# Performance work log

Measured on AMD Instinct MI355X. Metric: run time of the kernel, lower is better.

Reference implementation:

```python
import jax, jax.numpy as jnp
import numpy as np

# --- MLA config (DeepSeek-V3 style, scaled) ---
HIDDEN = 4096
N_HEADS = 32
Q_LORA = 1536
KV_LORA = 512
ROPE_D = 64
NOPE_D = 128
V_D = 128
Q_HEAD_D = NOPE_D + ROPE_D  # 192
EPS = 1e-6
SCALING = Q_HEAD_D ** (-0.5)
ROPE_THETA = 10000.0
B, S = 1, 2048


def rms_norm(x, w):
    var = jnp.mean(jnp.square(x.astype(jnp.float32)), axis=-1, keepdims=True)
    return (x * jax.lax.rsqrt(var + EPS)).astype(x.dtype) * w


def rotate_half(x):
    x1, x2 = jnp.split(x, 2, axis=-1)
    return jnp.concatenate([-x2, x1], axis=-1)


def apply_rope(x, cos, sin):
    # x: [B, H, S, ROPE_D]; cos/sin: [B, S, ROPE_D] -> unsqueeze head dim
    c = cos[:, None, :, :]
    s = sin[:, None, :, :]
    return x * c + rotate_half(x) * s


def setup_inputs() -> dict:
    key = jax.random.key(0)
    ks = jax.random.split(key, 8)
    hidden_states = jax.random.normal(ks[0], (B, S, HIDDEN), dtype=jnp.float32)
    # real RoPE tables
    inv_freq = 1.0 / (ROPE_THETA ** (np.arange(0, ROPE_D, 2, dtype=np.float32) / ROPE_D))
    t = np.arange(S, dtype=np.float32)
    freqs = np.outer(t, inv_freq)                      # [S, ROPE_D/2]
    emb = np.concatenate([freqs, freqs], axis=-1)      # [S, ROPE_D]
    cos = jnp.asarray(np.cos(emb))[None].repeat(B, 0)  # [B, S, ROPE_D]
    sin = jnp.asarray(np.sin(emb))[None].repeat(B, 0)
    scale = lambda fan_in: 1.0 / np.sqrt(fan_in)
    w_q_a = jax.random.normal(ks[1], (Q_LORA, HIDDEN), dtype=jnp.float32) * scale(HIDDEN)
    q_a_ln_w = jnp.ones((Q_LORA,), dtype=jnp.float32)
    w_q_b = jax.random.normal(ks[2], (N_HEADS * Q_HEAD_D, Q_LORA), dtype=jnp.float32) * scale(Q_LORA)
    w_kv_a = jax.random.normal(ks[3], (KV_LORA + ROPE_D, HIDDEN), dtype=jnp.float32) * scale(HIDDEN)
    kv_a_ln_w = jnp.ones((KV_LORA,), dtype=jnp.float32)
    w_kv_b = jax.random.normal(ks[4], (N_HEADS * (NOPE_D + V_D), KV_LORA), dtype=jnp.float32) * scale(KV_LORA)
    w_o = jax.random.normal(ks[5], (HIDDEN, N_HEADS * V_D), dtype=jnp.float32) * scale(N_HEADS * V_D)
    return {
        'hidden_states': hidden_states, 'cos': cos, 'sin': sin,
        'w_q_a': w_q_a, 'q_a_ln_w': q_a_ln_w, 'w_q_b': w_q_b,
        'w_kv_a': w_kv_a, 'kv_a_ln_w': kv_a_ln_w, 'w_kv_b': w_kv_b, 'w_o': w_o,
    }


def reference(hidden_states, cos, sin, w_q_a, q_a_ln_w, w_q_b, w_kv_a, kv_a_ln_w, w_kv_b, w_o):
    b, s, _ = hidden_states.shape
    # --- Q path: low-rank down + RMSNorm + up ---
    q_lat = rms_norm(hidden_states @ w_q_a.T, q_a_ln_w)              # [B,S,Q_LORA]
    q = (q_lat @ w_q_b.T).reshape(b, s, N_HEADS, Q_HEAD_D)
    q = q.transpose(0, 2, 1, 3)                                       # [B,H,S,Q_HEAD_D]
    q_nope, q_rot = q[..., :NOPE_D], q[..., NOPE_D:]                  # (note: source names swapped)
    # --- KV path: shared compressed latent + single rotary key ---
    ckv = hidden_states @ w_kv_a.T                                    # [B,S,KV_LORA+ROPE_D]
    k_lat, k_rot = ckv[..., :KV_LORA], ckv[..., KV_LORA:]
    kv = (rms_norm(k_lat, kv_a_ln_w) @ w_kv_b.T).reshape(b, s, N_HEADS, NOPE_D + V_D)
    kv = kv.transpose(0, 2, 1, 3)                                     # [B,H,S,NOPE_D+V_D]
    k_nope, v = kv[..., :NOPE_D], kv[..., NOPE_D:]
    k_rot = k_rot.reshape(b, 1, s, ROPE_D)                            # single rotary key head
    # --- partial RoPE on rotary slices ---
    q_rot = apply_rope(q_rot, cos, sin)
    k_rot = apply_rope(k_rot, cos, sin)
    k_rot = jnp.broadcast_to(k_rot, (b, N_HEADS, s, ROPE_D))
    query = jnp.concatenate([q_rot, q_nope], axis=-1)                 # [B,H,S,192]
    key = jnp.concatenate([k_rot, k_nope], axis=-1)                   # [B,H,S,192]
    # --- eager causal attention ---
    scores = jnp.einsum('bhqd,bhkd->bhqk', query, key) * SCALING
    causal = jnp.tril(jnp.ones((s, s), dtype=bool))
    scores = jnp.where(causal[None, None], scores, jnp.finfo(scores.dtype).min)
    probs = jax.nn.softmax(scores, axis=-1)
    attn = jnp.einsum('bhqk,bhkd->bhqd', probs, v)                    # [B,H,S,V_D]
    attn = attn.transpose(0, 2, 1, 3).reshape(b, s, N_HEADS * V_D)
    return attn @ w_o.T                                               # [B,S,HIDDEN]
```

## Files before the change

kernel.cpp:

```cpp
#include <hip/hip_runtime.h>

typedef unsigned short u16;
typedef u16 u16x4 __attribute__((ext_vector_type(4)));
typedef u16 u16x8 __attribute__((ext_vector_type(8)));
typedef float f32x4 __attribute__((ext_vector_type(4)));
typedef __bf16 bf16x8 __attribute__((ext_vector_type(8)));

#define S_LEN 2048
#define HIDDEN_D 4096
#define NHEADS 32
#define QLORA 1536
#define KVLORA 512
#define ROPED 64
#define NOPED 128
#define VDIM 128
#define QHD 192
#define SCALING_F 0.07216878364870323f

__device__ __forceinline__ u16 f2bf(float x) {
  union { float f; unsigned u; } v; v.f = x;
  unsigned r = v.u + 0x7fffu + ((v.u >> 16) & 1u);
  return (u16)(r >> 16);
}

__device__ __forceinline__ f32x4 mfma_bf16(u16x8 a, u16x8 b, f32x4 c) {
  return __builtin_amdgcn_mfma_f32_16x16x32_bf16(
      __builtin_bit_cast(bf16x8, a), __builtin_bit_cast(bf16x8, b), c, 0, 0, 0);
}

__global__ __launch_bounds__(256) void cvt_kernel(const float* __restrict__ in,
                                                  u16* __restrict__ out, int n4) {
  int i = blockIdx.x * 256 + threadIdx.x;
  if (i >= n4) return;
  f32x4 v = ((const f32x4*)in)[i];
  u16x4 o;
  o[0] = f2bf(v[0]); o[1] = f2bf(v[1]); o[2] = f2bf(v[2]); o[3] = f2bf(v[3]);
  ((u16x4*)out)[i] = o;
}

__global__ __launch_bounds__(256, 2) void gemm_kernel(
    const u16* __restrict__ A, const float* __restrict__ B, float* __restrict__ C,
    int M, int N, int K, int lda, int ldb, int ldc)
{
  __shared__ u16 sA[2][128 * 64];
  __shared__ u16 sB[2][128 * 64];
  const int tid = threadIdx.x;
  const int wid = tid >> 6, lane = tid & 63;
  const int lr = lane & 15, lg = lane >> 4;
  const int nbn = (N + 127) >> 7;
  const int bx = blockIdx.x % nbn, by = blockIdx.x / nbn;
  const int bm = by << 7, bn = bx << 7;
  const int wm = (wid >> 1) << 6, wn = (wid & 1) << 6;

  f32x4 acc[4][4] = {};
  u16x8 areg[4];
  f32x4 br0[4], br1[4];

  auto loadA = [&](int k0) {
#pragma unroll
    for (int i = 0; i < 4; ++i) {
      int chunk = i * 256 + tid;
      int row = chunk >> 3, c8 = chunk & 7;
      int gr = bm + row; if (gr >= M) gr = M - 1;
      areg[i] = *(const u16x8*)(A + (size_t)gr * lda + k0 + (c8 << 3));
    }
  };
  auto loadB = [&](int k0) {
#pragma unroll
    for (int i = 0; i < 4; ++i) {
      int chunk = i * 256 + tid;
      int n = chunk >> 3, c8 = chunk & 7;
      int gn = bn + n; if (gn >= N) gn = N - 1;
      const float* src = B + (size_t)gn * ldb + k0 + (c8 << 3);
      br0[i] = *(const f32x4*)src;
      br1[i] = *(const f32x4*)(src + 4);
    }
  };
  auto writeA = [&](int buf) {
#pragma unroll
    for (int i = 0; i < 4; ++i)
      *(u16x8*)&sA[buf][(i * 256 + tid) * 8] = areg[i];
  };
  auto writeB = [&](int buf) {
#pragma unroll
    for (int i = 0; i < 4; ++i) {
      u16x8 v;
      v[0] = f2bf(br0[i][0]); v[1] = f2bf(br0[i][1]);
      v[2] = f2bf(br0[i][2]); v[3] = f2bf(br0[i][3]);
      v[4] = f2bf(br1[i][0]); v[5] = f2bf(br1[i][1]);
      v[6] = f2bf(br1[i][2]); v[7] = f2bf(br1[i][3]);
      *(u16x8*)&sB[buf][(i * 256 + tid) * 8] = v;
    }
  };
  auto compute = [&](int buf) {
    const u16* pa = sA[buf];
    const u16* pb = sB[buf];
#pragma unroll
    for (int ks = 0; ks < 2; ++ks) {
      const int kof = ks * 32 + lg * 8;
      u16x8 av[4], bv[4];
#pragma unroll
      for (int m = 0; m < 4; ++m) av[m] = *(const u16x8*)&pa[(wm + m * 16 + lr) * 64 + kof];
#pragma unroll
      for (int n = 0; n < 4; ++n) bv[n] = *(const u16x8*)&pb[(wn + n * 16 + lr) * 64 + kof];
#pragma unroll
      for (int m = 0; m < 4; ++m)
#pragma unroll
        for (int n = 0; n < 4; ++n)
          acc[m][n] = mfma_bf16(av[m], bv[n], acc[m][n]);
    }
  };

  const int nk = K >> 6;
  loadA(0); loadB(0);
  writeA(0); writeB(0);
  __syncthreads();
  for (int t = 0; t < nk; ++t) {
    const int cur = t & 1;
    if (t + 1 < nk) { loadA((t + 1) << 6); loadB((t + 1) << 6); }
    compute(cur);
    if (t + 1 < nk) { writeA(cur ^ 1); writeB(cur ^ 1); }
    __syncthreads();
  }
#pragma unroll
  for (int m = 0; m < 4; ++m) {
    const int row0 = bm + wm + m * 16 + (lg << 2);
#pragma unroll
    for (int n = 0; n < 4; ++n) {
      const int col = bn + wn + n * 16 + lr;
      if (col < N) {
#pragma unroll
        for (int r = 0; r < 4; ++r)
          C[(size_t)(row0 + r) * ldc + col] = acc[m][n][r];
      }
    }
  }
}

__global__ __launch_bounds__(256) void rms_kernel(const float* __restrict__ X,
                                                  const float* __restrict__ w,
                                                  u16* __restrict__ out, int D) {
  const int row = blockIdx.x;
  const float* x = X + (size_t)row * D;
  __shared__ float sb[4];
  float ss = 0.f;
  for (int i = threadIdx.x * 4; i < D; i += 1024) {
    f32x4 v = *(const f32x4*)&x[i];
    ss += v[0] * v[0] + v[1] * v[1] + v[2] * v[2] + v[3] * v[3];
  }
#pragma unroll
  for (int off = 32; off >= 1; off >>= 1) ss += __shfl_xor(ss, off, 64);
  if ((threadIdx.x & 63) == 0) sb[threadIdx.x >> 6] = ss;
  __syncthreads();
  const float inv = rsqrtf((sb[0] + sb[1] + sb[2] + sb[3]) / (float)D + 1e-6f);
  u16* o = out + (size_t)row * D;
  for (int i = threadIdx.x * 4; i < D; i += 1024) {
    f32x4 v = *(const f32x4*)&x[i];
    f32x4 wv = *(const f32x4*)&w[i];
    u16x4 u;
    u[0] = f2bf(v[0] * inv * wv[0]); u[1] = f2bf(v[1] * inv * wv[1]);
    u[2] = f2bf(v[2] * inv * wv[2]); u[3] = f2bf(v[3] * inv * wv[3]);
    *(u16x4*)&o[i] = u;
  }
}

__global__ __launch_bounds__(256) void ckv_epi_kernel(const float* __restrict__ ckv,
    const float* __restrict__ w, const float* __restrict__ cosp, const float* __restrict__ sinp,
    u16* __restrict__ klatn, u16* __restrict__ krot) {
  const int s = blockIdx.x;
  const float* x = ckv + (size_t)s * 576;
  __shared__ float sb[4];
  const int i2 = threadIdx.x * 2;
  const float a = x[i2], b = x[i2 + 1];
  float ss = a * a + b * b;
#pragma unroll
  for (int off = 32; off >= 1; off >>= 1) ss += __shfl_xor(ss, off, 64);
  if ((threadIdx.x & 63) == 0) sb[threadIdx.x >> 6] = ss;
  __syncthreads();
  const float inv = rsqrtf((sb[0] + sb[1] + sb[2] + sb[3]) / 512.0f + 1e-6f);
  klatn[(size_t)s * 512 + i2]     = f2bf(a * inv * w[i2]);
  klatn[(size_t)s * 512 + i2 + 1] = f2bf(b * inv * w[i2 + 1]);
  if (threadIdx.x < 64) {
    const int d = threadIdx.x;
    const float xr = x[512 + d];
    const float rr = (d < 32) ? -x[512 + d + 32] : x[512 + d - 32];
    krot[(size_t)s * 64 + d] = f2bf(xr * cosp[s * 64 + d] + rr * sinp[s * 64 + d]);
  }
}

__global__ __launch_bounds__(256) void q_epi_kernel(const float* __restrict__ q_raw,
    const float* __restrict__ cosp, const float* __restrict__ sinp, u16* __restrict__ Qb) {
  const int s = blockIdx.x;
  const float* x = q_raw + (size_t)s * 6144;
  for (int idx = threadIdx.x; idx < 6144; idx += 256) {
    const int h = idx / 192, d = idx - h * 192;
    float v;
    if (d < 64) {
      const float xr = x[h * 192 + 128 + d];
      const float rr = (d < 32) ? -x[h * 192 + 160 + d] : x[h * 192 + 96 + d];
      v = xr * cosp[s * 64 + d] + rr * sinp[s * 64 + d];
    } else {
      v = x[h * 192 + d - 64];
    }
    Qb[((size_t)h * 2048 + s) * QHD + d] = f2bf(v * SCALING_F);
  }
}

__global__ __launch_bounds__(256) void kv_epi_kernel(const float* __restrict__ kv_raw,
    u16* __restrict__ Knope, u16* __restrict__ Vt) {
  const int h = blockIdx.x & 31, st = blockIdx.x >> 5;
  const int s0 = st << 6;
  __shared__ u16 tile[64][VDIM + 2];
  for (int i = 0; i < 32; ++i) {
    const int idx = i * 256 + threadIdx.x;
    const int r = idx >> 7, d = idx & 127;
    const float kn = kv_raw[(size_t)(s0 + r) * 8192 + h * 256 + d];
    Knope[((size_t)h * 2048 + s0 + r) * 128 + d] = f2bf(kn);
    tile[r][d] = f2bf(kv_raw[(size_t)(s0 + r) * 8192 + h * 256 + 128 + d]);
  }
  __syncthreads();
  for (int i = 0; i < 32; ++i) {
    const int idx = i * 256 + threadIdx.x;
    const int d = idx >> 6, r = idx & 63;
    Vt[((size_t)h * 128 + d) * 2048 + s0 + r] = tile[r][d];
  }
}

__global__ __launch_bounds__(256, 2) void flash_kernel(
    const u16* __restrict__ Qb, const u16* __restrict__ Krot,
    const u16* __restrict__ Knope, const u16* __restrict__ Vt,
    u16* __restrict__ attnb)
{
  const int h = blockIdx.x & 31, qt = blockIdx.x >> 5;
  const int q0 = qt << 7;
  __shared__ u16 sK[64][QHD];
  __shared__ u16 sV[VDIM][64];
  __shared__ u16 sP[4][32][64];
  const int tid = threadIdx.x;
  const int wid = tid >> 6, lane = tid & 63;
  const int lr = lane & 15, lg = lane >> 4;

  u16x8 qf[2][6];
#pragma unroll
  for (int m = 0; m < 2; ++m) {
    const int row = q0 + wid * 32 + m * 16 + lr;
#pragma unroll
    for (int kk = 0; kk < 6; ++kk)
      qf[m][kk] = *(const u16x8*)&Qb[((size_t)h * 2048 + row) * QHD + kk * 32 + lg * 8];
  }

  f32x4 acc[2][8] = {};
  float mx[2][4], ls[2][4];
#pragma unroll
  for (int m = 0; m < 2; ++m)
#pragma unroll
    for (int r = 0; r < 4; ++r) { mx[m][r] = -1e30f; ls[m][r] = 0.f; }

  const int nkv = q0 + 128;
  u16x8 kreg[6], vreg[4];

  auto loadKV = [&](int kv0) {
#pragma unroll
    for (int i = 0; i < 6; ++i) {
      const int chunk = i * 256 + tid;
      const int row = chunk / 24, cc = chunk % 24;
      const u16* src = (cc < 8)
          ? &Krot[(size_t)(kv0 + row) * 64 + cc * 8]
          : &Knope[((size_t)h * 2048 + kv0 + row) * 128 + (cc - 8) * 8];
      kreg[i] = *(const u16x8*)src;
    }
#pragma unroll
    for (int i = 0; i < 4; ++i) {
      const int chunk = i * 256 + tid;
      const int d = chunk >> 3, c = chunk & 7;
      vreg[i] = *(const u16x8*)&Vt[((size_t)h * VDIM + d) * 2048 + kv0 + c * 8];
    }
  };

  loadKV(0);
  for (int kv0 = 0; kv0 < nkv; kv0 += 64) {
    __syncthreads();
    u16* kbase = &sK[0][0];
#pragma unroll
    for (int i = 0; i < 6; ++i) *(u16x8*)&kbase[(size_t)(i * 256 + tid) * 8] = kreg[i];
    u16* vbase = &sV[0][0];
#pragma unroll
    for (int i = 0; i < 4; ++i) *(u16x8*)&vbase[(size_t)(i * 256 + tid) * 8] = vreg[i];
    __syncthreads();
    if (kv0 + 64 < nkv) loadKV(kv0 + 64);

    f32x4 sc[2][4] = {};
#pragma unroll
    for (int kk = 0; kk < 6; ++kk) {
      u16x8 bfr[4];
#pragma unroll
      for (int n = 0; n < 4; ++n) bfr[n] = *(const u16x8*)&sK[n * 16 + lr][kk * 32 + lg * 8];
#pragma unroll
      for (int m = 0; m < 2; ++m)
#pragma unroll
        for (int n = 0; n < 4; ++n)
          sc[m][n] = mfma_bf16(qf[m][kk], bfr[n], sc[m][n]);
    }

    if (kv0 + 63 > q0 + wid * 32) {
#pragma unroll
      for (int m = 0; m < 2; ++m)
#pragma unroll
        for (int n = 0; n < 4; ++n) {
          const int kv = kv0 + n * 16 + lr;
#pragma unroll
          for (int r = 0; r < 4; ++r) {
            const int rowq = q0 + wid * 32 + m * 16 + lg * 4 + r;
            if (kv > rowq) sc[m][n][r] = -1e30f;
          }
        }
    }

#pragma unroll
    for (int m = 0; m < 2; ++m) {
      float rs[4];
#pragma unroll
      for (int r = 0; r < 4; ++r) {
        float v = fmaxf(fmaxf(sc[m][0][r], sc[m][1][r]), fmaxf(sc[m][2][r], sc[m][3][r]));
#pragma unroll
        for (int off = 1; off < 16; off <<= 1) v = fmaxf(v, __shfl_xor(v, off, 64));
        const float mnew = fmaxf(mx[m][r], v);
        const float alpha = __expf(mx[m][r] - mnew);
        mx[m][r] = mnew;
        ls[m][r] *= alpha;
#pragma unroll
        for (int df = 0; df < 8; ++df) acc[m][df][r] *= alpha;
        rs[r] = 0.f;
      }
#pragma unroll
      for (int n = 0; n < 4; ++n)
#pragma unroll
        for (int r = 0; r < 4; ++r) {
          const float p = __expf(sc[m][n][r] - mx[m][r]);
          rs[r] += p;
          sP[wid][m * 16 + lg * 4 + r][n * 16 + lr] = f2bf(p);
        }
#pragma unroll
      for (int r = 0; r < 4; ++r) {
        float v = rs[r];
#pragma unroll
        for (int off = 1; off < 16; off <<= 1) v += __shfl_xor(v, off, 64);
        ls[m][r] += v;
      }
    }

#pragma unroll
    for (int ks = 0; ks < 2; ++ks) {
      u16x8 pf0 = *(const u16x8*)&sP[wid][lr][ks * 32 + lg * 8];
      u16x8 pf1 = *(const u16x8*)&sP[wid][16 + lr][ks * 32 + lg * 8];
#pragma unroll
      for (int df = 0; df < 8; ++df) {
        u16x8 vf = *(const u16x8*)&sV[df * 16 + lr][ks * 32 + lg * 8];
        acc[0][df] = mfma_bf16(pf0, vf, acc[0][df]);
        acc[1][df] = mfma_bf16(pf1, vf, acc[1][df]);
      }
    }
  }

#pragma unroll
  for (int m = 0; m < 2; ++m)
#pragma unroll
    for (int df = 0; df < 8; ++df) {
      const int col = h * 128 + df * 16 + lr;
#pragma unroll
      for (int r = 0; r < 4; ++r) {
        const int row = q0 + wid * 32 + m * 16 + lg * 4 + r;
        attnb[(size_t)row * 4096 + col] = f2bf(acc[m][df][r] / ls[m][r]);
      }
    }
}

extern "C" void kernel_launch(void* const* d_in, const int* in_sizes, int n_in,
                              void* d_out, int out_size, void* d_ws, size_t ws_size,
                              hipStream_t stream) {
  (void)in_sizes; (void)n_in; (void)out_size; (void)ws_size;
  const float* hidden  = (const float*)d_in[0];
  const float* cosp    = (const float*)d_in[1];
  const float* sinp    = (const float*)d_in[2];
  const float* w_q_a   = (const float*)d_in[3];
  const float* q_a_ln  = (const float*)d_in[4];
  const float* w_q_b   = (const float*)d_in[5];
  const float* w_kv_a  = (const float*)d_in[6];
  const float* kv_a_ln = (const float*)d_in[7];
  const float* w_kv_b  = (const float*)d_in[8];
  const float* w_o     = (const float*)d_in[9];
  float* out = (float*)d_out;

  char* p = (char*)d_ws;
  auto alloc = [&](size_t bytes) { char* r = p; p += (bytes + 255) & ~(size_t)255; return r; };
  u16* Hb    = (u16*)alloc((size_t)S_LEN * HIDDEN_D * 2);
  u16* qlatn = (u16*)alloc((size_t)S_LEN * QLORA * 2);
  u16* klatn = (u16*)alloc((size_t)S_LEN * KVLORA * 2);
  u16* krot  = (u16*)alloc((size_t)S_LEN * ROPED * 2);
  u16* Qb    = (u16*)alloc((size_t)NHEADS * S_LEN * QHD * 2);
  u16* Knope = (u16*)alloc((size_t)NHEADS * S_LEN * NOPED * 2);
  u16* Vt    = (u16*)alloc((size_t)NHEADS * VDIM * S_LEN * 2);
  u16* attnb = (u16*)alloc((size_t)S_LEN * 4096 * 2);
  float* raw = (float*)alloc((size_t)S_LEN * 8192 * 4);
  float* qlat_raw = raw;
  float* ckv_raw  = raw + (size_t)S_LEN * QLORA;
  float* q_raw    = raw;
  float* kv_raw   = raw;

  cvt_kernel<<<(S_LEN * HIDDEN_D / 4 + 255) / 256, 256, 0, stream>>>(hidden, Hb, S_LEN * HIDDEN_D / 4);
  gemm_kernel<<<16 * 12, 256, 0, stream>>>(Hb, w_q_a, qlat_raw, 2048, 1536, 4096, 4096, 4096, 1536);
  gemm_kernel<<<16 * 5, 256, 0, stream>>>(Hb, w_kv_a, ckv_raw, 2048, 576, 4096, 4096, 4096, 576);
  rms_kernel<<<2048, 256, 0, stream>>>(qlat_raw, q_a_ln, qlatn, 1536);
  ckv_epi_kernel<<<2048, 256, 0, stream>>>(ckv_raw, kv_a_ln, cosp, sinp, klatn, krot);
  gemm_kernel<<<16 * 48, 256, 0, stream>>>(qlatn, w_q_b, q_raw, 2048, 6144, 1536, 1536, 1536, 6144);
  q_epi_kernel<<<2048, 256, 0, stream>>>(q_raw, cosp, sinp, Qb);
  gemm_kernel<<<16 * 64, 256, 0, stream>>>(klatn, w_kv_b, kv_raw, 2048, 8192, 512, 512, 512, 8192);
  kv_epi_kernel<<<1024, 256, 0, stream>>>(kv_raw, Knope, Vt);
  flash_kernel<<<512, 256, 0, stream>>>(Qb, krot, Knope, Vt, attnb);
  gemm_kernel<<<16 * 32, 256, 0, stream>>>(attnb, w_o, out, 2048, 4096, 4096, 4096, 4096, 4096);
}
```

Measured before the change: 680.3 us.

## Swizzle flash-attention LDS layouts, balance causal tiles, raise MFMA priority

The K, V and P shared-memory tiles switch to flat arrays addressed with an XOR swizzle on 16-byte chunks. This is meant to remove LDS bank conflicts on the strided row reads that feed the MFMA operands. Query tiles are now assigned to blocks in a paired order (early and late tiles) so that causal work is spread more evenly across concurrently scheduled blocks. s_setprio is raised around the MFMA loops to favour matrix issue across waves, at the cost of extra index arithmetic per access.

After: 976.8 us. +43.6%, slower.

```diff
diff --git a/kernel.cpp b/kernel.cpp
--- a/kernel.cpp
+++ b/kernel.cpp
@@ -231,11 +231,14 @@
     const u16* __restrict__ Knope, const u16* __restrict__ Vt,
     u16* __restrict__ attnb)
 {
-  const int h = blockIdx.x & 31, qt = blockIdx.x >> 5;
+  const int bid = blockIdx.x;
+  const int h = bid & 31;
+  const int q8 = (bid & 255) >> 5;
+  const int qt = (bid >> 8) ? (15 - 2 * q8) : (2 * q8);
   const int q0 = qt << 7;
-  __shared__ u16 sK[64][QHD];
-  __shared__ u16 sV[VDIM][64];
-  __shared__ u16 sP[4][32][64];
+  __shared__ u16 sK[64 * QHD];
+  __shared__ u16 sV[VDIM * 64];
+  __shared__ u16 sP[4 * 32 * 64];
   const int tid = threadIdx.x;
   const int wid = tid >> 6, lane = tid & 63;
   const int lr = lane & 15, lg = lane >> 4;
@@ -244,9 +247,10 @@
 #pragma unroll
   for (int m = 0; m < 2; ++m) {
     const int row = q0 + wid * 32 + m * 16 + lr;
+    const u16* qp = &Qb[((size_t)h * 2048 + row) * QHD];
 #pragma unroll
     for (int kk = 0; kk < 6; ++kk)
-      qf[m][kk] = *(const u16x8*)&Qb[((size_t)h * 2048 + row) * QHD + kk * 32 + lg * 8];
+      qf[m][kk] = *(const u16x8*)&qp[kk * 32 + lg * 8];
   }
 
   f32x4 acc[2][8] = {};
@@ -278,29 +282,44 @@
   };
 
   loadKV(0);
+  const int pbase = wid * 8192;
   for (int kv0 = 0; kv0 < nkv; kv0 += 64) {
     __syncthreads();
-    u16* kbase = &sK[0][0];
-#pragma unroll
-    for (int i = 0; i < 6; ++i) *(u16x8*)&kbase[(size_t)(i * 256 + tid) * 8] = kreg[i];
-    u16* vbase = &sV[0][0];
-#pragma unroll
-    for (int i = 0; i < 4; ++i) *(u16x8*)&vbase[(size_t)(i * 256 + tid) * 8] = vreg[i];
+#pragma unroll
+    for (int i = 0; i < 6; ++i) {
+      const int chunk = i * 256 + tid;
+      const int row = chunk / 24, cc = chunk % 24;
+      int b = row * 384 + cc * 16; b ^= (row & 7) << 4;
+      *(u16x8*)&sK[b >> 1] = kreg[i];
+    }
+#pragma unroll
+    for (int i = 0; i < 4; ++i) {
+      const int chunk = i * 256 + tid;
+      const int row = chunk >> 3, cc = chunk & 7;
+      int b = row * 128 + cc * 16; b ^= (row & 7) << 4;
+      *(u16x8*)&sV[b >> 1] = vreg[i];
+    }
     __syncthreads();
     if (kv0 + 64 < nkv) loadKV(kv0 + 64);
 
     f32x4 sc[2][4] = {};
+    __builtin_amdgcn_s_setprio(1);
 #pragma unroll
     for (int kk = 0; kk < 6; ++kk) {
       u16x8 bfr[4];
 #pragma unroll
-      for (int n = 0; n < 4; ++n) bfr[n] = *(const u16x8*)&sK[n * 16 + lr][kk * 32 + lg * 8];
+      for (int n = 0; n < 4; ++n) {
+        const int row = n * 16 + lr;
+        int b = row * 384 + kk * 64 + lg * 16; b ^= (row & 7) << 4;
+        bfr[n] = *(const u16x8*)&sK[b >> 1];
+      }
 #pragma unroll
       for (int m = 0; m < 2; ++m)
 #pragma unroll
         for (int n = 0; n < 4; ++n)
           sc[m][n] = mfma_bf16(qf[m][kk], bfr[n], sc[m][n]);
     }
+    __builtin_amdgcn_s_setprio(0);
 
     if (kv0 + 63 > q0 + wid * 32) {
 #pragma unroll
@@ -338,7 +357,9 @@
         for (int r = 0; r < 4; ++r) {
           const float p = __expf(sc[m][n][r] - mx[m][r]);
           rs[r] += p;
-          sP[wid][m * 16 + lg * 4 + r][n * 16 + lr] = f2bf(p);
+          const int prow = m * 16 + lg * 4 + r;
+          int b = prow * 128 + (n * 16 + lr) * 2; b ^= (prow & 7) << 4;
+          sP[(wid * 4096 + b) >> 1] = f2bf(p);
         }
 #pragma unroll
       for (int r = 0; r < 4; ++r) {
@@ -349,17 +370,23 @@
       }
     }
 
+    __builtin_amdgcn_s_setprio(1);
 #pragma unroll
     for (int ks = 0; ks < 2; ++ks) {
-      u16x8 pf0 = *(const u16x8*)&sP[wid][lr][ks * 32 + lg * 8];
-      u16x8 pf1 = *(const u16x8*)&sP[wid][16 + lr][ks * 32 + lg * 8];
+      int b0 = lr * 128 + ks * 64 + lg * 16; b0 ^= (lr & 7) << 4;
+      int b1 = (16 + lr) * 128 + ks * 64 + lg * 16; b1 ^= (lr & 7) << 4;
+      u16x8 pf0 = *(const u16x8*)&sP[(wid * 4096 + b0) >> 1];
+      u16x8 pf1 = *(const u16x8*)&sP[(wid * 4096 + b1) >> 1];
 #pragma unroll
       for (int df = 0; df < 8; ++df) {
-        u16x8 vf = *(const u16x8*)&sV[df * 16 + lr][ks * 32 + lg * 8];
+        const int vrow = df * 16 + lr;
+        int vb = vrow * 128 + ks * 64 + lg * 16; vb ^= (vrow & 7) << 4;
+        u16x8 vf = *(const u16x8*)&sV[vb >> 1];
         acc[0][df] = mfma_bf16(pf0, vf, acc[0][df]);
         acc[1][df] = mfma_bf16(pf1, vf, acc[1][df]);
       }
     }
+    __builtin_amdgcn_s_setprio(0);
   }
 
 #pragma unroll
```
